# Performance work log

Hardware: AMD Instinct MI355X
Metric: run time of the kernel (lower is better)

## Reference

```python
import jax, jax.numpy as jnp
import numpy as np

B, T, C = 2, 2048, 1024
NHEADS = 16
HEAD_DIM = C // NHEADS  # 64
THETA = 10000.0
SCALE_BASE = 512.0
GN_EPS = 1e-5


def setup_inputs() -> dict:
    key = jax.random.key(0)
    ks = jax.random.split(key, 4)
    s = 0.02
    return {
        "x": jax.random.normal(ks[0], (B, T, C), jnp.float32),
        "w_qkv": jax.random.normal(ks[1], (3 * C, C), jnp.float32) * s,
        "w_gated": jax.random.normal(ks[2], (C, C), jnp.float32) * s,
        "w_proj": jax.random.normal(ks[3], (C, C), jnp.float32) * s,
        "gn_weight": jnp.ones((C,), jnp.float32),
        "gn_bias": jnp.zeros((C,), jnp.float32),
    }


def _rotate_half(x):
    # pairs are adjacent/interleaved: (d r) with r=2
    x1 = x[..., 0::2]
    x2 = x[..., 1::2]
    return jnp.stack([-x2, x1], axis=-1).reshape(x.shape)


def _rope_xpos(q, k, T):
    # lucidrains rotary_embedding_torch with use_xpos=True
    d = q.shape[-1]
    half = jnp.arange(0, d, 2, dtype=jnp.float32)
    inv_freq = 1.0 / (THETA ** (half / d))
    t = jnp.arange(T, dtype=jnp.float32)
    freqs = t[:, None] * inv_freq[None, :]          # [T, d/2]
    freqs = jnp.repeat(freqs, 2, axis=-1)           # [T, d] interleaved
    scale_vec = (half + 0.4 * d) / (1.4 * d)        # [d/2]
    power = (t - T // 2) / SCALE_BASE               # [T]
    scale = scale_vec[None, :] ** power[:, None]    # [T, d/2]
    scale = jnp.repeat(scale, 2, axis=-1)           # [T, d]
    cos, sin = jnp.cos(freqs), jnp.sin(freqs)
    q = q * (cos * scale) + _rotate_half(q) * (sin * scale)
    k = k * (cos / scale) + _rotate_half(k) * (sin / scale)
    return q, k


def _decay_mask(T):
    # gamma_h = 1 - 2^(-5-h); mask[h,i,j] = gamma_h^(i-j) for i>=j else 0
    gamma = 1.0 - 2.0 ** (-5.0 - jnp.arange(NHEADS, dtype=jnp.float32))
    idx = jnp.arange(T)
    diff = idx[:, None] - idx[None, :]              # [T, T]
    causal = diff >= 0
    expn = jnp.where(causal, diff, 0).astype(jnp.float32)
    return jnp.where(causal[None], gamma[:, None, None] ** expn[None], 0.0)


def reference(x, w_qkv, w_gated, w_proj, gn_weight, gn_bias):
    Bx, Tx, Cx = x.shape
    qkv = x @ w_qkv.T                               # [B,T,3C]
    q, k, v = jnp.split(qkv, 3, axis=-1)
    def to_heads(u):
        return u.reshape(Bx, Tx, NHEADS, HEAD_DIM).transpose(0, 2, 1, 3)
    q, k, v = to_heads(q), to_heads(k), to_heads(v)  # [B,H,T,D]
    q, k = _rope_xpos(q, k, Tx)
    mask = _decay_mask(Tx)                           # [H,T,T]
    scores = jnp.einsum('bhtd,bhsd->bhts', q, k) * (HEAD_DIM ** -0.5)
    scores = scores * mask[None]
    y = jnp.einsum('bhts,bhsd->bhtd', scores, v)     # [B,H,T,D]
    y = y.transpose(0, 2, 1, 3).reshape(Bx, Tx, Cx)  # [B,T,C]
    # GroupNorm over (B, C, T) with num_groups = NHEADS: normalize each
    # group's (C/H channels x T positions) jointly.
    yt = y.transpose(0, 2, 1).reshape(Bx, NHEADS, HEAD_DIM, Tx)
    mean = yt.mean(axis=(2, 3), keepdims=True)
    var = yt.var(axis=(2, 3), keepdims=True)
    yn = (yt - mean) / jnp.sqrt(var + GN_EPS)
    yn = yn.reshape(Bx, Cx, Tx)
    yn = yn * gn_weight[None, :, None] + gn_bias[None, :, None]
    yn = yn.transpose(0, 2, 1)                       # [B,T,C]
    out = jax.nn.silu(x @ w_gated.T) * yn
    return out @ w_proj.T
```

## Files before the change

kernel.cpp:

```cpp
#include <hip/hip_runtime.h>

typedef __attribute__((ext_vector_type(8))) short bf16x8;
typedef __attribute__((ext_vector_type(4))) float f32x4;
typedef __attribute__((ext_vector_type(16))) float f32x16;
typedef __attribute__((ext_vector_type(2))) unsigned short u16x2;
typedef __attribute__((ext_vector_type(4))) unsigned short u16x4;
typedef __attribute__((ext_vector_type(2))) unsigned int u32x2;

static constexpr int kB = 2;
static constexpr int kT = 2048;
static constexpr int kC = 1024;
static constexpr int kH = 16;
static constexpr int kD = 64;
static constexpr int kNC = 16;

__device__ inline unsigned short f2bf(float f) {
    unsigned int u = __float_as_uint(f);
    u += 0x7FFFu + ((u >> 16) & 1u);
    return (unsigned short)(u >> 16);
}
__device__ inline float bf2f(unsigned short u) {
    return __uint_as_float(((unsigned int)u) << 16);
}

#define GLDS16(g, s)                                                            \
    __builtin_amdgcn_global_load_lds(                                           \
        (const __attribute__((address_space(1))) unsigned int*)(g),             \
        (__attribute__((address_space(3))) unsigned int*)(s), 16, 0, 0)

__global__ __launch_bounds__(256) void cvt_bf16(const float* __restrict__ in,
                                                unsigned short* __restrict__ out, int n) {
    int i = (blockIdx.x * 256 + threadIdx.x) * 4;
    if (i >= n) return;
    float4 v = *(const float4*)(in + i);
    u16x4 o;
    o[0] = f2bf(v.x); o[1] = f2bf(v.y); o[2] = f2bf(v.z); o[3] = f2bf(v.w);
    *(u16x4*)(out + i) = o;
}

__global__ __launch_bounds__(256) void rope_tables(float2* __restrict__ qtab,
                                                   float2* __restrict__ ktab) {
    int idx = blockIdx.x * 256 + threadIdx.x;
    if (idx >= kT * 32) return;
    int t = idx >> 5, i = idx & 31;
    float half = 2.0f * (float)i;
    float inv_freq = powf(10000.0f, -half / 64.0f);
    float fr = (float)t * inv_freq;
    float sv = (half + 0.4f * 64.0f) / (1.4f * 64.0f);
    float p = ((float)t - 1024.0f) / 512.0f;
    float scl = powf(sv, p);
    float c = cosf(fr), s = sinf(fr);
    qtab[idx] = make_float2(c * scl, s * scl);
    ktab[idx] = make_float2(c / scl, s / scl);
}

__global__ __launch_bounds__(256) void dec_tables(float* __restrict__ decq,
                                                  float* __restrict__ deck) {
    int idx = blockIdx.x * 256 + threadIdx.x;
    if (idx >= kH * 128) return;
    int h = idx >> 7, tt = idx & 127;
    float log2g = log2f(1.0f - exp2f(-5.0f - (float)h));
    decq[idx] = 0.125f * exp2f(log2g * (float)tt);
    deck[idx] = exp2f(-log2g * (float)tt);
}

__global__ __launch_bounds__(256) void gemm_qkvg(const unsigned short* __restrict__ A,
                                                 const unsigned short* __restrict__ Bm,
                                                 unsigned short* __restrict__ qb,
                                                 unsigned short* __restrict__ kbuf,
                                                 unsigned short* __restrict__ vtb,
                                                 unsigned short* __restrict__ gbuf) {
    constexpr int K = 1024;
    __shared__ __align__(16) unsigned short Al[128 * 64];
    __shared__ __align__(16) unsigned short Bl[128 * 64];
    char* ab = (char*)Al;
    char* bb = (char*)Bl;
    const int tid = threadIdx.x;
    const int l = tid & 63, w = tid >> 6;
    const int wr = w >> 1, wc = w & 1;
    const int tm = blockIdx.y * 128, tn = blockIdx.x * 128;
    const int ri = l >> 3;
    const int su = (l & 7) ^ (ri & 7);

    f32x4 zero4 = {0.0f, 0.0f, 0.0f, 0.0f};
    f32x4 acc[4][4];
#pragma unroll
    for (int m = 0; m < 4; m++)
#pragma unroll
        for (int n = 0; n < 4; n++) acc[m][n] = zero4;

    for (int kt = 0; kt < K; kt += 64) {
#pragma unroll
        for (int c = w; c < 32; c += 4) {
            if (c < 16) {
                const unsigned short* src = A + (size_t)(tm + c * 8 + ri) * K + kt + su * 8;
                GLDS16(src, ab + c * 1024);
            } else {
                int cb = c - 16;
                const unsigned short* src = Bm + (size_t)(tn + cb * 8 + ri) * K + kt + su * 8;
                GLDS16(src, bb + cb * 1024);
            }
        }
        __syncthreads();
#pragma unroll
        for (int ks = 0; ks < 2; ks++) {
            bf16x8 af[4], bfr[4];
            int kbyte = ks * 64 + (l >> 4) * 16;
#pragma unroll
            for (int m = 0; m < 4; m++) {
                int row = wr * 64 + m * 16 + (l & 15);
                af[m] = *(const bf16x8*)(ab + row * 128 + (kbyte ^ ((row & 7) << 4)));
            }
#pragma unroll
            for (int n = 0; n < 4; n++) {
                int row = wc * 64 + n * 16 + (l & 15);
                bfr[n] = *(const bf16x8*)(bb + row * 128 + (kbyte ^ ((row & 7) << 4)));
            }
#pragma unroll
            for (int m = 0; m < 4; m++)
#pragma unroll
                for (int n = 0; n < 4; n++)
                    acc[m][n] = __builtin_amdgcn_mfma_f32_16x16x32_bf16(af[m], bfr[n], acc[m][n], 0, 0, 0);
        }
        __syncthreads();
    }

    if (tn < 2048) {
        const bool isq = (tn < 1024);
        unsigned short* dst = isq ? qb : kbuf;
        const int colbase = isq ? tn : (tn - 1024);
#pragma unroll
        for (int n = 0; n < 4; n++) {
            int col = colbase + wc * 64 + n * 16 + (l & 15);
            int h = col >> 6;
            int d = col & 63;
#pragma unroll
            for (int m = 0; m < 4; m++) {
#pragma unroll
                for (int r = 0; r < 4; r++) {
                    int row = tm + wr * 64 + m * 16 + (l >> 4) * 4 + r;
                    int b = row >> 11, t = row & 2047;
                    unsigned int ub = f2bf(acc[m][n][r]);
                    unsigned int pb = (unsigned int)__shfl_xor((int)ub, 1);
                    if (!(l & 1)) {
                        unsigned int packed = (ub & 0xFFFFu) | (pb << 16);
                        *(unsigned int*)(dst + ((size_t)(b * 16 + h) * 2048 + t) * 64 + d) = packed;
                    }
                }
            }
        }
    } else if (tn < 3072) {
#pragma unroll
        for (int m = 0; m < 4; m++)
#pragma unroll
            for (int n = 0; n < 4; n++) {
                int col2 = (tn - 2048) + wc * 64 + n * 16 + (l & 15);
                int rowb = tm + wr * 64 + m * 16 + (l >> 4) * 4;
                int b = rowb >> 11, t = rowb & 2047;
                u16x4 o;
#pragma unroll
                for (int r = 0; r < 4; r++) o[r] = f2bf(acc[m][n][r]);
                *(u16x4*)(vtb + ((size_t)(b * 1024 + col2)) * 2048 + t) = o;
            }
    } else {
#pragma unroll
        for (int m = 0; m < 4; m++)
#pragma unroll
            for (int n = 0; n < 4; n++)
#pragma unroll
                for (int r = 0; r < 4; r++) {
                    int row = tm + wr * 64 + m * 16 + (l >> 4) * 4 + r;
                    int col3 = (tn - 3072) + wc * 64 + n * 16 + (l & 15);
                    float v = acc[m][n][r];
                    float sv2 = v / (1.0f + expf(-v));
                    gbuf[(size_t)row * 1024 + col3] = f2bf(sv2);
                }
    }
}

__global__ __launch_bounds__(256) void rope_qkt(unsigned short* __restrict__ qb,
                                                unsigned short* __restrict__ kbuf,
                                                unsigned short* __restrict__ ktb,
                                                const float2* __restrict__ qtab,
                                                const float2* __restrict__ ktab,
                                                const float* __restrict__ decq,
                                                const float* __restrict__ deck) {
    __shared__ unsigned short tile[64][72];
    const int bh = blockIdx.x;
    const int tt = blockIdx.y * 64;
    const int h = bh & 15;
    const int tl = threadIdx.x >> 2;
    const int du = (threadIdx.x & 3) * 16;
    const int t = tt + tl;
    const float dq = decq[h * 128 + (t & 127)];
    const float dk = deck[h * 128 + (t & 127)];

    {
        unsigned short* qrow = qb + ((size_t)bh * kT + t) * kD + du;
        bf16x8 a0 = *(const bf16x8*)(qrow);
        bf16x8 a1 = *(const bf16x8*)(qrow + 8);
        bf16x8 o0, o1;
#pragma unroll
        for (int j = 0; j < 4; ++j) {
            float2 cs = qtab[t * 32 + (du >> 1) + j];
            float x0 = bf2f((unsigned short)a0[2 * j]);
            float x1 = bf2f((unsigned short)a0[2 * j + 1]);
            o0[2 * j] = (short)f2bf((x0 * cs.x - x1 * cs.y) * dq);
            o0[2 * j + 1] = (short)f2bf((x1 * cs.x + x0 * cs.y) * dq);
            float2 cs2 = qtab[t * 32 + (du >> 1) + 4 + j];
            float y0 = bf2f((unsigned short)a1[2 * j]);
            float y1 = bf2f((unsigned short)a1[2 * j + 1]);
            o1[2 * j] = (short)f2bf((y0 * cs2.x - y1 * cs2.y) * dq);
            o1[2 * j + 1] = (short)f2bf((y1 * cs2.x + y0 * cs2.y) * dq);
        }
        *(bf16x8*)(qrow) = o0;
        *(bf16x8*)(qrow + 8) = o1;
    }
    {
        unsigned short* krow = kbuf + ((size_t)bh * kT + t) * kD + du;
        bf16x8 a0 = *(const bf16x8*)(krow);
        bf16x8 a1 = *(const bf16x8*)(krow + 8);
        bf16x8 o0, o1;
#pragma unroll
        for (int j = 0; j < 4; ++j) {
            float2 cs = ktab[t * 32 + (du >> 1) + j];
            float x0 = bf2f((unsigned short)a0[2 * j]);
            float x1 = bf2f((unsigned short)a0[2 * j + 1]);
            o0[2 * j] = (short)f2bf((x0 * cs.x - x1 * cs.y) * dk);
            o0[2 * j + 1] = (short)f2bf((x1 * cs.x + x0 * cs.y) * dk);
            float2 cs2 = ktab[t * 32 + (du >> 1) + 4 + j];
            float y0 = bf2f((unsigned short)a1[2 * j]);
            float y1 = bf2f((unsigned short)a1[2 * j + 1]);
            o1[2 * j] = (short)f2bf((y0 * cs2.x - y1 * cs2.y) * dk);
            o1[2 * j + 1] = (short)f2bf((y1 * cs2.x + y0 * cs2.y) * dk);
        }
        *(bf16x8*)(krow) = o0;
        *(bf16x8*)(krow + 8) = o1;
#pragma unroll
        for (int e = 0; e < 8; ++e) {
            tile[tl][du + e] = (unsigned short)o0[e];
            tile[tl][du + 8 + e] = (unsigned short)o1[e];
        }
    }
    __syncthreads();
    {
        int dd = threadIdx.x >> 2;
        int tb2 = (threadIdx.x & 3) * 16;
        bf16x8 o0, o1;
#pragma unroll
        for (int e = 0; e < 8; ++e) {
            o0[e] = (short)tile[tb2 + e][dd];
            o1[e] = (short)tile[tb2 + 8 + e][dd];
        }
        unsigned short* drow = ktb + ((size_t)bh * kD + dd) * kT + tt + tb2;
        *(bf16x8*)(drow) = o0;
        *(bf16x8*)(drow + 8) = o1;
    }
}

__global__ __launch_bounds__(256) void chunk_m(const unsigned short* __restrict__ ktb,
                                               const unsigned short* __restrict__ vtb,
                                               unsigned short* __restrict__ Mt) {
    __shared__ __align__(16) unsigned short Ktl[64 * 128];
    __shared__ __align__(16) unsigned short Vtl[64 * 128];
    const int tid = threadIdx.x, l = tid & 63, w = tid >> 6;
    const int bh = blockIdx.x, c = blockIdx.y, h = bh & 15;
    const int ql = l & 31, hi5 = l >> 5;
    char* kp = (char*)Ktl;
    char* vp = (char*)Vtl;
#pragma unroll
    for (int j = 0; j < 4; ++j) {
        int ch = w * 4 + j;
        int row = ch * 4 + (l >> 4);
        int u = (l & 15) ^ (row & 15);
        GLDS16(ktb + ((size_t)bh * kD + row) * kT + c * 128 + u * 8, kp + ch * 1024);
        GLDS16(vtb + ((size_t)bh * kD + row) * kT + c * 128 + u * 8, vp + ch * 1024);
    }
    __syncthreads();
    const int iw = w >> 1, jw = w & 1;
    f32x16 acc;
#pragma unroll
    for (int r = 0; r < 16; ++r) acc[r] = 0.0f;
#pragma unroll
    for (int sk = 0; sk < 8; ++sk) {
        int rowa = iw * 32 + ql;
        int rowb = jw * 32 + ql;
        bf16x8 av = *(const bf16x8*)(vp + rowa * 256 + 16 * ((2 * sk + hi5) ^ (rowa & 15)));
        bf16x8 bk = *(const bf16x8*)(kp + rowb * 256 + 16 * ((2 * sk + hi5) ^ (rowb & 15)));
        acc = __builtin_amdgcn_mfma_f32_32x32x16_bf16(av, bk, acc, 0, 0, 0);
    }
    float log2g = log2f(1.0f - exp2f(-5.0f - (float)h));
    float gC = exp2f(128.0f * log2g);
    unsigned short* mo = Mt + ((size_t)(bh * kNC + c)) * 4096;
#pragma unroll
    for (int r = 0; r < 16; ++r) {
        int row = iw * 32 + (r & 3) + 8 * (r >> 2) + 4 * hi5;
        int col = jw * 32 + ql;
        mo[row * 64 + col] = f2bf(acc[r] * gC);
    }
}

__global__ __launch_bounds__(256) void chunk_states(const unsigned short* __restrict__ Mt,
                                                    unsigned short* __restrict__ St) {
    const int bh = blockIdx.x, c = blockIdx.y, h = bh & 15;
    const int tid = threadIdx.x;
    float log2g = log2f(1.0f - exp2f(-5.0f - (float)h));
    float gC = exp2f(128.0f * log2g);
    float acc[16];
#pragma unroll
    for (int e = 0; e < 16; ++e) acc[e] = 0.0f;
    for (int j = 0; j < c; ++j) {
        const unsigned short* m = Mt + ((size_t)(bh * kNC + j)) * 4096;
#pragma unroll
        for (int k = 0; k < 4; ++k) {
            u16x4 v = *(const u16x4*)(m + (k * 256 + tid) * 4);
#pragma unroll
            for (int e = 0; e < 4; ++e) {
                float f = bf2f(v[e]);
                acc[k * 4 + e] = acc[k * 4 + e] * gC + f;
            }
        }
    }
    unsigned short* so = St + ((size_t)(bh * kNC + c)) * 4096;
#pragma unroll
    for (int k = 0; k < 4; ++k) {
        u16x4 o;
#pragma unroll
        for (int e = 0; e < 4; ++e) o[e] = f2bf(acc[k * 4 + e]);
        *(u16x4*)(so + (k * 256 + tid) * 4) = o;
    }
}

__global__ __launch_bounds__(512) void chunk_attn(const unsigned short* __restrict__ qb,
                                                  const unsigned short* __restrict__ kb,
                                                  const unsigned short* __restrict__ vtb,
                                                  const unsigned short* __restrict__ St,
                                                  unsigned short* __restrict__ yb,
                                                  float* __restrict__ part) {
    __shared__ __align__(16) unsigned short Kt[128 * 64];
    __shared__ __align__(16) unsigned short Vt[64 * 128];
    __shared__ __align__(16) unsigned short Ss[64 * 64];
    __shared__ __align__(16) unsigned short Pl[8 * 32 * 64];
    __shared__ float red[16];
    const int tid = threadIdx.x, l = tid & 63, w = tid >> 6;
    const int bh = blockIdx.x, c = blockIdx.y;
    const int qw = w >> 1, dw = w & 1;
    const int ql = l & 31, hi5 = l >> 5;
    char* kp = (char*)Kt;
    char* vp = (char*)Vt;
    char* sp = (char*)Ss;
    char* pw = (char*)Pl + w * 4096;

#pragma unroll
    for (int j = 0; j < 2; ++j) {
        int ch = w * 2 + j;
        int row = ch * 8 + (l >> 3);
        int u = (l & 7) ^ (row & 7);
        GLDS16(kb + ((size_t)bh * kT + c * 128 + row) * kD + u * 8, kp + ch * 1024);
    }
#pragma unroll
    for (int j = 0; j < 2; ++j) {
        int ch = w * 2 + j;
        int row = ch * 4 + (l >> 4);
        int u = (l & 15) ^ (row & 15);
        GLDS16(vtb + ((size_t)bh * kD + row) * kT + c * 128 + u * 8, vp + ch * 1024);
    }
    {
        int row = w * 8 + (l >> 3);
        int u = (l & 7) ^ (row & 7);
        GLDS16(St + ((size_t)(bh * kNC + c)) * 4096 + row * 64 + u * 8, sp + w * 1024);
    }
    bf16x8 aq[4];
    {
        const unsigned short* qrow = qb + ((size_t)bh * kT + c * 128 + qw * 32 + ql) * kD + hi5 * 8;
#pragma unroll
        for (int dk = 0; dk < 4; ++dk) aq[dk] = *(const bf16x8*)(qrow + dk * 16);
    }
    __syncthreads();

    f32x16 acc;
#pragma unroll
    for (int r = 0; r < 16; ++r) acc[r] = 0.0f;
    const int qidx = qw * 32 + ql;

#pragma unroll
    for (int p = 0; p < 2; ++p) {
        f32x16 sA, sB;
#pragma unroll
        for (int r = 0; r < 16; ++r) { sA[r] = 0.0f; sB[r] = 0.0f; }
#pragma unroll
        for (int dk = 0; dk < 4; ++dk) {
            int rowa = (2 * p) * 32 + ql;
            int rowb = (2 * p + 1) * 32 + ql;
            bf16x8 ka = *(const bf16x8*)(kp + rowa * 128 + 16 * ((2 * dk + hi5) ^ (rowa & 7)));
            bf16x8 kb2 = *(const bf16x8*)(kp + rowb * 128 + 16 * ((2 * dk + hi5) ^ (rowb & 7)));
            sA = __builtin_amdgcn_mfma_f32_32x32x16_bf16(ka, aq[dk], sA, 0, 0, 0);
            sB = __builtin_amdgcn_mfma_f32_32x32x16_bf16(kb2, aq[dk], sB, 0, 0, 0);
        }
#pragma unroll
        for (int sb2 = 0; sb2 < 2; ++sb2) {
            int sbase = (2 * p + sb2) * 32 + 4 * hi5;
#pragma unroll
            for (int m = 0; m < 4; ++m) {
                float v0, v1, v2, v3;
                {
                    int s0i = sbase + 8 * m;
                    float x0 = sb2 ? sB[4 * m + 0] : sA[4 * m + 0];
                    float x1 = sb2 ? sB[4 * m + 1] : sA[4 * m + 1];
                    float x2 = sb2 ? sB[4 * m + 2] : sA[4 * m + 2];
                    float x3 = sb2 ? sB[4 * m + 3] : sA[4 * m + 3];
                    v0 = (qidx >= s0i + 0) ? x0 : 0.0f;
                    v1 = (qidx >= s0i + 1) ? x1 : 0.0f;
                    v2 = (qidx >= s0i + 2) ? x2 : 0.0f;
                    v3 = (qidx >= s0i + 3) ? x3 : 0.0f;
                }
                unsigned int lo, hi;
                asm("v_cvt_pk_bf16_f32 %0, %1, %2" : "=v"(lo) : "v"(v0), "v"(v1));
                asm("v_cvt_pk_bf16_f32 %0, %1, %2" : "=v"(hi) : "v"(v2), "v"(v3));
                u32x2 pr; pr[0] = lo; pr[1] = hi;
                *(u32x2*)(pw + ql * 128 + (((sb2 * 4 + m) * 16) ^ ((ql & 7) << 4)) + hi5 * 8) = pr;
            }
        }
#pragma unroll
        for (int kki = 0; kki < 4; ++kki) {
            bf16x8 ap = *(const bf16x8*)(pw + ql * 128 + 16 * ((2 * kki + hi5) ^ (ql & 7)));
            int rowv = dw * 32 + ql;
            bf16x8 bv = *(const bf16x8*)(vp + rowv * 256 + 16 * ((2 * (4 * p + kki) + hi5) ^ (rowv & 15)));
            acc = __builtin_amdgcn_mfma_f32_32x32x16_bf16(ap, bv, acc, 0, 0, 0);
        }
    }
#pragma unroll
    for (int dk = 0; dk < 4; ++dk) {
        int rows = dw * 32 + ql;
        bf16x8 bs = *(const bf16x8*)(sp + rows * 128 + 16 * ((2 * dk + hi5) ^ (rows & 7)));
        acc = __builtin_amdgcn_mfma_f32_32x32x16_bf16(aq[dk], bs, acc, 0, 0, 0);
    }
    float s = 0.0f, s2 = 0.0f;
#pragma unroll
    for (int r = 0; r < 16; ++r) {
        int row = c * 128 + qw * 32 + (r & 3) + 8 * (r >> 2) + 4 * hi5;
        int col = dw * 32 + ql;
        unsigned short ub = f2bf(acc[r]);
        yb[((size_t)bh * kT + row) * kD + col] = ub;
        float f = bf2f(ub);
        s += f; s2 += f * f;
    }
#pragma unroll
    for (int o = 32; o > 0; o >>= 1) {
        s += __shfl_down(s, o);
        s2 += __shfl_down(s2, o);
    }
    if (l == 0) { red[w * 2] = s; red[w * 2 + 1] = s2; }
    __syncthreads();
    if (tid == 0) {
        float S = 0.0f, S2 = 0.0f;
#pragma unroll
        for (int i = 0; i < 8; i++) { S += red[2 * i]; S2 += red[2 * i + 1]; }
        part[((size_t)bh * kNC + c) * 2] = S;
        part[((size_t)bh * kNC + c) * 2 + 1] = S2;
    }
}

__global__ __launch_bounds__(64) void gn_fin(const float* __restrict__ part,
                                             float* __restrict__ stats) {
    int bh = threadIdx.x;
    if (bh >= kB * kH) return;
    float S = 0.0f, S2 = 0.0f;
#pragma unroll
    for (int i = 0; i < kNC; i++) {
        S += part[(bh * kNC + i) * 2];
        S2 += part[(bh * kNC + i) * 2 + 1];
    }
    const float inv = 1.0f / (float)(kT * kD);
    float mean = S * inv;
    float var = S2 * inv - mean * mean;
    stats[2 * bh] = mean;
    stats[2 * bh + 1] = rsqrtf(var + 1e-5f);
}

__global__ __launch_bounds__(256) void gemm_proj(const unsigned short* __restrict__ A,
                                                 const unsigned short* __restrict__ Bm,
                                                 float* __restrict__ Cf,
                                                 int N, int K) {
    __shared__ __align__(16) unsigned short Al[128 * 64];
    __shared__ __align__(16) unsigned short Bl[128 * 64];
    char* ab = (char*)Al;
    char* bb = (char*)Bl;
    const int tid = threadIdx.x;
    const int l = tid & 63, w = tid >> 6;
    const int wr = w >> 1, wc = w & 1;
    const int tm = blockIdx.y * 128, tn = blockIdx.x * 128;
    const int ri = l >> 3;
    const int su = (l & 7) ^ (ri & 7);

    f32x4 zero4 = {0.0f, 0.0f, 0.0f, 0.0f};
    f32x4 acc[4][4];
#pragma unroll
    for (int m = 0; m < 4; m++)
#pragma unroll
        for (int n = 0; n < 4; n++) acc[m][n] = zero4;

    for (int kt = 0; kt < K; kt += 64) {
#pragma unroll
        for (int c = w; c < 32; c += 4) {
            if (c < 16) {
                const unsigned short* src = A + (size_t)(tm + c * 8 + ri) * K + kt + su * 8;
                GLDS16(src, ab + c * 1024);
            } else {
                int cb = c - 16;
                const unsigned short* src = Bm + (size_t)(tn + cb * 8 + ri) * K + kt + su * 8;
                GLDS16(src, bb + cb * 1024);
            }
        }
        __syncthreads();
#pragma unroll
        for (int ks = 0; ks < 2; ks++) {
            bf16x8 af[4], bfr[4];
            int kbyte = ks * 64 + (l >> 4) * 16;
#pragma unroll
            for (int m = 0; m < 4; m++) {
                int row = wr * 64 + m * 16 + (l & 15);
                af[m] = *(const bf16x8*)(ab + row * 128 + (kbyte ^ ((row & 7) << 4)));
            }
#pragma unroll
            for (int n = 0; n < 4; n++) {
                int row = wc * 64 + n * 16 + (l & 15);
                bfr[n] = *(const bf16x8*)(bb + row * 128 + (kbyte ^ ((row & 7) << 4)));
            }
#pragma unroll
            for (int m = 0; m < 4; m++)
#pragma unroll
                for (int n = 0; n < 4; n++)
                    acc[m][n] = __builtin_amdgcn_mfma_f32_16x16x32_bf16(af[m], bfr[n], acc[m][n], 0, 0, 0);
        }
        __syncthreads();
    }
#pragma unroll
    for (int m = 0; m < 4; m++)
#pragma unroll
        for (int n = 0; n < 4; n++)
#pragma unroll
            for (int r = 0; r < 4; r++) {
                int row = tm + wr * 64 + m * 16 + (l >> 4) * 4 + r;
                int col = tn + wc * 64 + n * 16 + (l & 15);
                Cf[(size_t)row * N + col] = acc[m][n][r];
            }
}

__global__ __launch_bounds__(256) void fuse_z(const unsigned short* __restrict__ gb,
                                              const unsigned short* __restrict__ yb,
                                              const float* __restrict__ stats,
                                              const float* __restrict__ gnw,
                                              const float* __restrict__ gnb,
                                              unsigned short* __restrict__ z) {
    int idx = blockIdx.x * 256 + threadIdx.x;
    int row = idx >> 8;
    int c = (idx & 255) << 2;
    int b = row >> 11, t = row & 2047;
    int h = c >> 6, d = c & 63;
    int bh = b * kH + h;
    u16x4 gv = *(const u16x4*)(gb + (size_t)row * kC + c);
    u16x4 yv = *(const u16x4*)(yb + (((size_t)bh * kT) + t) * kD + d);
    float mean = stats[2 * bh], rstd = stats[2 * bh + 1];
    float4 wv = *(const float4*)(gnw + c);
    float4 bv = *(const float4*)(gnb + c);
    u16x4 o;
    o[0] = f2bf(bf2f(gv[0]) * ((bf2f(yv[0]) - mean) * rstd * wv.x + bv.x));
    o[1] = f2bf(bf2f(gv[1]) * ((bf2f(yv[1]) - mean) * rstd * wv.y + bv.y));
    o[2] = f2bf(bf2f(gv[2]) * ((bf2f(yv[2]) - mean) * rstd * wv.z + bv.z));
    o[3] = f2bf(bf2f(gv[3]) * ((bf2f(yv[3]) - mean) * rstd * wv.w + bv.w));
    *(u16x4*)(z + (size_t)row * kC + c) = o;
}

extern "C" void kernel_launch(void* const* d_in, const int* in_sizes, int n_in,
                              void* d_out, int out_size, void* d_ws, size_t ws_size,
                              hipStream_t stream) {
    const float* x = (const float*)d_in[0];
    const float* w_qkv = (const float*)d_in[1];
    const float* w_gated = (const float*)d_in[2];
    const float* w_proj = (const float*)d_in[3];
    const float* gnw = (const float*)d_in[4];
    const float* gnb = (const float*)d_in[5];
    float* out = (float*)d_out;
    char* ws = (char*)d_ws;

    unsigned short* xb      = (unsigned short*)(ws + 0);
    unsigned short* wqkvb   = (unsigned short*)(ws + 8388608);
    unsigned short* wgatedb = (unsigned short*)(ws + 14680064);
    unsigned short* wprojb  = (unsigned short*)(ws + 16777216);
    unsigned short* qb      = (unsigned short*)(ws + 18874368);
    unsigned short* kbuf    = (unsigned short*)(ws + 27262976);
    unsigned short* vtb     = (unsigned short*)(ws + 35651584);
    unsigned short* zb      = (unsigned short*)(ws + 44040192);
    float* part  = (float*)(ws + 44040192);
    float* stats = (float*)(ws + 52428800);
    float2* qtab = (float2*)(ws + 52429056);
    float2* ktab = (float2*)(ws + 52953344);
    float*  decq = (float*)(ws + 53477632);
    float*  deck = (float*)(ws + 53485824);
    unsigned short* Mt  = (unsigned short*)(ws + 52429056);
    unsigned short* St  = (unsigned short*)(ws + 56623360);
    unsigned short* yb  = (unsigned short*)(ws + 60817664);
    unsigned short* gbuf= (unsigned short*)(ws + 69206272);
    unsigned short* ktb = (unsigned short*)(ws + 77594880);

    cvt_bf16<<<4096, 256, 0, stream>>>(x, xb, kB * kT * kC);
    cvt_bf16<<<3072, 256, 0, stream>>>(w_qkv, wqkvb, 3 * kC * kC);
    cvt_bf16<<<1024, 256, 0, stream>>>(w_gated, wgatedb, kC * kC);
    cvt_bf16<<<1024, 256, 0, stream>>>(w_proj, wprojb, kC * kC);
    rope_tables<<<256, 256, 0, stream>>>(qtab, ktab);
    dec_tables<<<8, 256, 0, stream>>>(decq, deck);

    gemm_qkvg<<<dim3(32, 32), 256, 0, stream>>>(xb, wqkvb, qb, kbuf, vtb, gbuf);

    rope_qkt<<<dim3(kB * kH, kT / 64), 256, 0, stream>>>(qb, kbuf, ktb, qtab, ktab, decq, deck);

    chunk_m<<<dim3(kB * kH, kNC), 256, 0, stream>>>(ktb, vtb, Mt);
    chunk_states<<<dim3(kB * kH, kNC), 256, 0, stream>>>(Mt, St);
    chunk_attn<<<dim3(kB * kH, kNC), 512, 0, stream>>>(qb, kbuf, vtb, St, yb, part);

    gn_fin<<<1, 64, 0, stream>>>(part, stats);

    fuse_z<<<4096, 256, 0, stream>>>(gbuf, yb, stats, gnw, gnb, zb);

    gemm_proj<<<dim3(kC / 128, 4096 / 128), 256, 0, stream>>>(zb, wprojb, out, kC, kC);
}
```

Before: 134.3 us.

## Double-buffer LDS in QKV/gate and projection GEMMs with async prefetch

Both GEMM kernels now keep two LDS buffers and issue the global-to-LDS loads for the next K tile before computing on the current one. Explicit vmcnt waits and raw barriers replace __syncthreads, so memory latency can overlap with MFMA work. The gate epilogue also pairs adjacent lanes with a shuffle to write two bf16 values per store. LDS use doubles to 64KB per block, which may reduce occupancy, and the hand-counted vmcnt(8) has to match the number of loads issued per stage.

```diff
diff --git a/kernel.cpp b/kernel.cpp
--- a/kernel.cpp
+++ b/kernel.cpp
@@ -27,6 +27,11 @@
     __builtin_amdgcn_global_load_lds(                                           \
         (const __attribute__((address_space(1))) unsigned int*)(g),             \
         (__attribute__((address_space(3))) unsigned int*)(s), 16, 0, 0)
+
+#define WAITVM8() asm volatile("s_waitcnt vmcnt(8)" ::: "memory")
+#define WAITVM0() asm volatile("s_waitcnt vmcnt(0)" ::: "memory")
+#define WAITLG() asm volatile("s_waitcnt lgkmcnt(0)" ::: "memory")
+#define SBAR() __builtin_amdgcn_s_barrier()
 
 __global__ __launch_bounds__(256) void cvt_bf16(const float* __restrict__ in,
                                                 unsigned short* __restrict__ out, int n) {
@@ -71,10 +76,8 @@
                                                  unsigned short* __restrict__ vtb,
                                                  unsigned short* __restrict__ gbuf) {
     constexpr int K = 1024;
-    __shared__ __align__(16) unsigned short Al[128 * 64];
-    __shared__ __align__(16) unsigned short Bl[128 * 64];
-    char* ab = (char*)Al;
-    char* bb = (char*)Bl;
+    __shared__ __align__(16) unsigned short Al[2][128 * 64];
+    __shared__ __align__(16) unsigned short Bl[2][128 * 64];
     const int tid = threadIdx.x;
     const int l = tid & 63, w = tid >> 6;
     const int wr = w >> 1, wc = w & 1;
@@ -89,19 +92,33 @@
 #pragma unroll
         for (int n = 0; n < 4; n++) acc[m][n] = zero4;
 
-    for (int kt = 0; kt < K; kt += 64) {
-#pragma unroll
-        for (int c = w; c < 32; c += 4) {
-            if (c < 16) {
-                const unsigned short* src = A + (size_t)(tm + c * 8 + ri) * K + kt + su * 8;
-                GLDS16(src, ab + c * 1024);
-            } else {
-                int cb = c - 16;
-                const unsigned short* src = Bm + (size_t)(tn + cb * 8 + ri) * K + kt + su * 8;
-                GLDS16(src, bb + cb * 1024);
-            }
-        }
-        __syncthreads();
+    auto STAGE = [&](int kt, int pb) {
+        char* ab = (char*)Al[pb];
+        char* bb = (char*)Bl[pb];
+#pragma unroll
+        for (int c = w; c < 16; c += 4) {
+            const unsigned short* src = A + (size_t)(tm + c * 8 + ri) * K + kt + su * 8;
+            GLDS16(src, ab + c * 1024);
+        }
+#pragma unroll
+        for (int c = w; c < 16; c += 4) {
+            const unsigned short* src = Bm + (size_t)(tn + c * 8 + ri) * K + kt + su * 8;
+            GLDS16(src, bb + c * 1024);
+        }
+    };
+
+    STAGE(0, 0);
+    for (int i = 0; i < 16; ++i) {
+        const int cur = i & 1;
+        if (i + 1 < 16) {
+            STAGE((i + 1) * 64, cur ^ 1);
+            WAITVM8();
+        } else {
+            WAITVM0();
+        }
+        SBAR();
+        char* ab = (char*)Al[cur];
+        char* bb = (char*)Bl[cur];
 #pragma unroll
         for (int ks = 0; ks < 2; ks++) {
             bf16x8 af[4], bfr[4];
@@ -122,7 +139,8 @@
                 for (int n = 0; n < 4; n++)
                     acc[m][n] = __builtin_amdgcn_mfma_f32_16x16x32_bf16(af[m], bfr[n], acc[m][n], 0, 0, 0);
         }
-        __syncthreads();
+        WAITLG();
+        SBAR();
     }
 
     if (tn < 2048) {
@@ -164,17 +182,24 @@
             }
     } else {
 #pragma unroll
-        for (int m = 0; m < 4; m++)
-#pragma unroll
-            for (int n = 0; n < 4; n++)
+        for (int n = 0; n < 4; n++) {
+            int col3 = (tn - 3072) + wc * 64 + n * 16 + (l & 15);
+#pragma unroll
+            for (int m = 0; m < 4; m++) {
 #pragma unroll
                 for (int r = 0; r < 4; r++) {
                     int row = tm + wr * 64 + m * 16 + (l >> 4) * 4 + r;
-                    int col3 = (tn - 3072) + wc * 64 + n * 16 + (l & 15);
                     float v = acc[m][n][r];
                     float sv2 = v / (1.0f + expf(-v));
-                    gbuf[(size_t)row * 1024 + col3] = f2bf(sv2);
+                    unsigned int ub = f2bf(sv2);
+                    unsigned int pb = (unsigned int)__shfl_xor((int)ub, 1);
+                    if (!(l & 1)) {
+                        unsigned int packed = (ub & 0xFFFFu) | (pb << 16);
+                        *(unsigned int*)(gbuf + (size_t)row * 1024 + col3) = packed;
+                    }
                 }
+            }
+        }
     }
 }
 
@@ -482,16 +507,15 @@
                                                  const unsigned short* __restrict__ Bm,
                                                  float* __restrict__ Cf,
                                                  int N, int K) {
-    __shared__ __align__(16) unsigned short Al[128 * 64];
-    __shared__ __align__(16) unsigned short Bl[128 * 64];
-    char* ab = (char*)Al;
-    char* bb = (char*)Bl;
+    __shared__ __align__(16) unsigned short Al[2][128 * 64];
+    __shared__ __align__(16) unsigned short Bl[2][128 * 64];
     const int tid = threadIdx.x;
     const int l = tid & 63, w = tid >> 6;
     const int wr = w >> 1, wc = w & 1;
     const int tm = blockIdx.y * 128, tn = blockIdx.x * 128;
     const int ri = l >> 3;
     const int su = (l & 7) ^ (ri & 7);
+    const int NK = K >> 6;
 
     f32x4 zero4 = {0.0f, 0.0f, 0.0f, 0.0f};
     f32x4 acc[4][4];
@@ -500,19 +524,33 @@
 #pragma unroll
         for (int n = 0; n < 4; n++) acc[m][n] = zero4;
 
-    for (int kt = 0; kt < K; kt += 64) {
-#pragma unroll
-        for (int c = w; c < 32; c += 4) {
-            if (c < 16) {
-                const unsigned short* src = A + (size_t)(tm + c * 8 + ri) * K + kt + su * 8;
-                GLDS16(src, ab + c * 1024);
-            } else {
-                int cb = c - 16;
-                const unsigned short* src = Bm + (size_t)(tn + cb * 8 + ri) * K + kt + su * 8;
-                GLDS16(src, bb + cb * 1024);
-            }
-        }
-        __syncthreads();
+    auto STAGE = [&](int kt, int pb) {
+        char* ab = (char*)Al[pb];
+        char* bb = (char*)Bl[pb];
+#pragma unroll
+        for (int c = w; c < 16; c += 4) {
+            const unsigned short* src = A + (size_t)(tm + c * 8 + ri) * K + kt + su * 8;
+            GLDS16(src, ab + c * 1024);
+        }
+#pragma unroll
+        for (int c = w; c < 16; c += 4) {
+            const unsigned short* src = Bm + (size_t)(tn + c * 8 + ri) * K + kt + su * 8;
+            GLDS16(src, bb + c * 1024);
+        }
+    };
+
+    STAGE(0, 0);
+    for (int i = 0; i < NK; ++i) {
+        const int cur = i & 1;
+        if (i + 1 < NK) {
+            STAGE((i + 1) * 64, cur ^ 1);
+            WAITVM8();
+        } else {
+            WAITVM0();
+        }
+        SBAR();
+        char* ab = (char*)Al[cur];
+        char* bb = (char*)Bl[cur];
 #pragma unroll
         for (int ks = 0; ks < 2; ks++) {
             bf16x8 af[4], bfr[4];
@@ -533,7 +571,8 @@
                 for (int n = 0; n < 4; n++)
                     acc[m][n] = __builtin_amdgcn_mfma_f32_16x16x32_bf16(af[m], bfr[n], acc[m][n], 0, 0, 0);
         }
-        __syncthreads();
+        WAITLG();
+        SBAR();
     }
 #pragma unroll
     for (int m = 0; m < 4; m++)
```

Measured after the change: 138.7 us. 1.03x slower.
